# Optimization experiments

Hardware: AMD Instinct MI355X
Metric: run time of the kernel (lower is better)

Reference implementation:

```python
import jax, jax.numpy as jnp
import numpy as np

V = 1.0e10           # large init value for non-seed pixels (FastGeodis v)
LAMB = 0.0           # lamb=0 => pure Euclidean raster-scan distance
ITERS = 2            # FastGeodis iterations
THRESH = 0.7         # binarize_map threshold
TOPO_WEIGHT = 0.005
TOPO_WINDOW = 64
EPS = 1e-6
BIG = 1e20


def _sweep_down(dist, image):
    # One top-down raster sweep of the FastGeodis up-down pass.
    # dist, image: [H, W]. Row r updates from row r-1 at col offsets {-1,0,+1}
    # with squared spatial distances {2,1,2}; lamb weights the intensity term.
    W = dist.shape[1]
    sp2 = (2.0, 1.0, 2.0)

    def step(carry, xs):
        pd, pi = carry          # previous-row distance / intensity, [W]
        d_row, i_row = xs
        pd_pad = jnp.pad(pd, 1, constant_values=BIG)
        pi_pad = jnp.pad(pi, 1, constant_values=0.0)
        new = d_row
        for k in range(3):
            p = pd_pad[k:k + W]
            q = i_row - pi_pad[k:k + W]
            new = jnp.minimum(new, p + jnp.sqrt(sp2[k] + LAMB * q * q))
        return (new, i_row), new

    (_, _), rest = jax.lax.scan(step, (dist[0], image[0]), (dist[1:], image[1:]))
    return jnp.concatenate([dist[:1], rest], axis=0)


def _updown(dist, image):
    dist = _sweep_down(dist, image)
    dist = _sweep_down(dist[::-1], image[::-1])[::-1]
    return dist


def generalised_geodesic2d(image, softmask):
    # image: intensity map [H,W]; softmask: [H,W]; dist init = V * softmask.
    dist = V * softmask
    for _ in range(ITERS):
        dist = _updown(dist, image)
        dist = _updown(dist.T, image.T).T
    return dist


def calculate_edt(inp):
    # Original: softmask = inp, intensity image = 1 - inp (mask_pt = 1 - image_pt).
    return generalised_geodesic2d(1.0 - inp, inp)


def _global_norm(x):
    return (x - x.min()) / (x.max() - x.min() + EPS)


def _topo_loss(p, t, window):
    # Persistence-style matching proxy: within each non-overlapping window,
    # match level-set values of pred and target by sorting (0-dim persistence
    # birth/death values of the filtration are order statistics of the window)
    # and penalize squared differences of matched values.
    H, W = p.shape
    nh, nw = H // window, W // window

    def win_sort(x):
        x = x.reshape(nh, window, nw, window).transpose(0, 2, 1, 3)
        return jnp.sort(x.reshape(nh * nw, window * window), axis=-1)

    return jnp.mean((win_sort(p) - win_sort(t)) ** 2)


def _per_item(pred_i, target_i):
    # pred_i/target_i: [C, H, W]; pred already remapped to [0, 1]
    bin_pred = (pred_i >= THRESH).astype(jnp.float32)
    comb_pred = jnp.max(bin_pred, axis=0)        # combine_channels
    comb_tgt = jnp.max(target_i, axis=0)
    edt_p = _global_norm(calculate_edt(1.0 - comb_pred))
    edt_t = _global_norm(calculate_edt(1.0 - comb_tgt))
    return _topo_loss(edt_p, edt_t, TOPO_WINDOW)


def setup_inputs():
    key = jax.random.key(0)
    k1, k2 = jax.random.split(key)
    B, C, H, W = 16, 3, 512, 512
    pred = jax.random.normal(k1, (B, C, H, W), dtype=jnp.float32)  # model output in ~[-1,1]
    # target: binary multi-channel cell masks (sparse foreground)
    target = (jax.random.uniform(k2, (B, C, H, W)) > 0.8).astype(jnp.float32)
    return {"pred": pred, "target": target}


def reference(pred, target):
    pred01 = (pred + 1.0) / 2.0
    losses = jax.vmap(_per_item)(pred01.astype(jnp.float32), target.astype(jnp.float32))
    mean_loss = losses.mean()
    return (mean_loss * TOPO_WEIGHT, mean_loss)
```

## Files before the change

kernel.cpp:

```cpp
#include <hip/hip_runtime.h>

#define BIGF 1e20f
#define VF   1e10f

constexpr float SQ2 = 1.41421356237309515f;

__device__ __forceinline__ float dpp_left(float x)
{
    int o = __builtin_amdgcn_update_dpp(0x60AD78ECu , __float_as_int(x),
                                        0x138, 0xF, 0xF, false);
    return __int_as_float(o);
}
__device__ __forceinline__ float dpp_right(float x)
{
    int o = __builtin_amdgcn_update_dpp(0x60AD78ECu , __float_as_int(x),
                                        0x130, 0xF, 0xF, false);
    return __int_as_float(o);
}
template<int CTRL>
__device__ __forceinline__ float qdpp(float x)
{
    return __int_as_float(__builtin_amdgcn_update_dpp(0, __float_as_int(x),
                                                      CTRL, 0xF, 0xF, true));
}
__device__ __forceinline__ float fmed3(float a, float b, float c)
{
    return __builtin_amdgcn_fmed3f(a, b, c);
}

__device__ __forceinline__ void load_row8(const float* __restrict__ M, int r, int c0, float v[8])
{
    const float4* q = (const float4*)(M + ((long)r << 9) + c0);
    float4 a = q[0], b = q[1];
    v[0] = a.x; v[1] = a.y; v[2] = a.z; v[3] = a.w;
    v[4] = b.x; v[5] = b.y; v[6] = b.z; v[7] = b.w;
}
__device__ __forceinline__ void store_row8(float* __restrict__ M, int r, int c0, const float v[8])
{
    float4* q = (float4*)(M + ((long)r << 9) + c0);
    q[0] = make_float4(v[0], v[1], v[2], v[3]);
    q[1] = make_float4(v[4], v[5], v[6], v[7]);
}

__device__ __forceinline__ void step8(const float cur[8], const float p[8], float nv[8])
{
    float left  = dpp_left(p[7]);
    float right = dpp_right(p[0]);
    #pragma unroll
    for (int j = 0; j < 8; ++j) {
        float l  = (j == 0) ? left  : p[j - 1];
        float rr = (j == 7) ? right : p[j + 1];
        nv[j] = fminf(fminf(cur[j], p[j] + 1.0f), fminf(l, rr) + SQ2);
    }
}

__global__ __launch_bounds__(256) void k_init(const float* __restrict__ pred,
                                              const float* __restrict__ tgt,
                                              float* __restrict__ bufA,
                                              float* __restrict__ acc,
                                              unsigned* __restrict__ count,
                                              float* __restrict__ minmax)
{
    if (blockIdx.x == 0 && threadIdx.x == 0) { *acc = 0.0f; *count = 0u; }
    if (blockIdx.x == 0 && threadIdx.x < 64)
        minmax[threadIdx.x] = (threadIdx.x & 1) ? 0.0f : BIGF;

    int r = blockIdx.x & 7;
    int k = blockIdx.x >> 3;
    int b = r + 8 * (k >> 10);
    int pix = (k & 1023) * 256 + threadIdx.x;
    long base = (long)b * 3 * 262144 + pix;

    float p0 = pred[base], p1 = pred[base + 262144], p2 = pred[base + 2 * 262144];
    bool fgP = ((p0 + 1.0f) * 0.5f >= 0.7f) ||
               ((p1 + 1.0f) * 0.5f >= 0.7f) ||
               ((p2 + 1.0f) * 0.5f >= 0.7f);

    float t0 = tgt[base], t1 = tgt[base + 262144], t2 = tgt[base + 2 * 262144];
    float mt = fmaxf(fmaxf(t0, t1), t2);

    bufA[(long)b * 262144 + pix]        = fgP ? 0.0f : VF;
    bufA[(long)(16 + b) * 262144 + pix] = VF * (1.0f - mt);
}

__global__ __launch_bounds__(64) void k_p1d(const float* __restrict__ X0,
                                            float* __restrict__ Cb)
{
    int bi = blockIdx.x, m = bi >> 4, w = bi & 15;
    const float* X = X0 + ((long)m << 18);
    int c0 = (int)threadIdx.x << 3, a = w << 5;
    float p[8]; load_row8(X, a, c0, p);
    float buf[8][8];
    #pragma unroll
    for (int k = 1; k <= 7; ++k) load_row8(X, a + k, c0, buf[k & 7]);
    #pragma unroll
    for (int i = 1; i < 32; ++i) {
        if (i + 7 < 32) load_row8(X, a + i + 7, c0, buf[(i + 7) & 7]);
        float nv[8]; step8(buf[i & 7], p, nv);
        #pragma unroll
        for (int j = 0; j < 8; ++j) p[j] = nv[j];
    }
    float4* o = (float4*)(Cb + m * 8192 + w * 512 + c0);
    o[0] = make_float4(p[0], p[1], p[2], p[3]);
    o[1] = make_float4(p[4], p[5], p[6], p[7]);
}

__device__ __forceinline__ void combine(float* __restrict__ bwp, float* __restrict__ part,
                                        int wdst, int wsrc, int t, int wave, int lane,
                                        const float wreg[8])
{
    const float* bs = bwp + wsrc * 576;
    if (wave <= 8) {
        int base = lane * 8 + 8 * wave;
        float W[16];
        float4 W0 = *(const float4*)(bs + base);
        float4 W1 = *(const float4*)(bs + base + 4);
        W[0]=W0.x; W[1]=W0.y; W[2]=W0.z; W[3]=W0.w;
        W[4]=W1.x; W[5]=W1.y; W[6]=W1.z; W[7]=W1.w;
        float acc[8];
        if (wave < 8) {
            float4 W2 = *(const float4*)(bs + base + 8);
            float4 W3 = *(const float4*)(bs + base + 12);
            W[8]=W2.x; W[9]=W2.y; W[10]=W2.z; W[11]=W2.w;
            W[12]=W3.x; W[13]=W3.y; W[14]=W3.z; W[15]=W3.w;
            #pragma unroll
            for (int j = 0; j < 8; ++j) acc[j] = W[j] + wreg[0];
            #pragma unroll
            for (int dt = 1; dt < 8; ++dt)
                #pragma unroll
                for (int j = 0; j < 8; ++j)
                    acc[j] = fminf(acc[j], W[j + dt] + wreg[dt]);
        } else {
            #pragma unroll
            for (int j = 0; j < 8; ++j) acc[j] = W[j] + wreg[0];
        }
        float4* pp = (float4*)(part + wave * 512 + lane * 8);
        pp[0] = make_float4(acc[0], acc[1], acc[2], acc[3]);
        pp[1] = make_float4(acc[4], acc[5], acc[6], acc[7]);
    }
    __syncthreads();
    if (t < 512) {
        float r = bwp[wdst * 576 + 32 + t];
        #pragma unroll
        for (int p2 = 0; p2 < 9; ++p2) r = fminf(r, part[p2 * 512 + t]);
        bwp[wdst * 576 + 32 + t] = r;
    }
    __syncthreads();
}

__global__ __launch_bounds__(1024) void k_comb(float* __restrict__ Cb, int dir)
{
    __shared__ __align__(16) float bwp[16 * 576];
    __shared__ __align__(16) float part[9 * 512];
    __shared__ float wgt[72];
    int m = blockIdx.x, t = threadIdx.x, wave = t >> 6, lane = t & 63, c0 = lane << 3;
    float* Cm = Cb + m * 8192;

    bwp[wave * 576 + ((lane < 32) ? lane : lane + 512)] = BIGF;
    *(float4*)(bwp + wave * 576 + 32 + c0)     = *(const float4*)(Cm + wave * 512 + c0);
    *(float4*)(bwp + wave * 576 + 32 + c0 + 4) = *(const float4*)(Cm + wave * 512 + c0 + 4);
    if (t < 65) { int d = t - 32; int ad = d < 0 ? -d : d; wgt[t] = ad * SQ2 + (float)(32 - ad); }
    __syncthreads();
    float wreg[8];
    #pragma unroll
    for (int dt = 0; dt < 8; ++dt) wreg[dt] = BIGF;
    if (wave < 8) {
        #pragma unroll
        for (int dt = 0; dt < 8; ++dt) wreg[dt] = wgt[wave * 8 + dt];
    } else if (wave == 8) wreg[0] = wgt[64];

    #pragma unroll 1
    for (int i = 0; i < 15; ++i) {
        int w2 = (dir > 0) ? (1 + i) : (14 - i);
        combine(bwp, part, w2, w2 - dir, t, wave, lane, wreg);
    }
    *(float4*)(Cm + wave * 512 + c0)     = *(const float4*)(bwp + wave * 576 + 32 + c0);
    *(float4*)(Cm + wave * 512 + c0 + 4) = *(const float4*)(bwp + wave * 576 + 32 + c0 + 4);
}

__global__ __launch_bounds__(64) void k_p3d1u(const float* __restrict__ X0,
                                              float* __restrict__ Y0,
                                              const float* __restrict__ Cb,
                                              float* __restrict__ Db)
{
    __shared__ __align__(16) float stash[31 * 512];
    int bi = blockIdx.x, m = bi >> 4, w = bi & 15;
    const float* X = X0 + ((long)m << 18);
    float* Y = Y0 + ((long)m << 18);
    const int L = threadIdx.x;
    int c0 = L << 3, a = w << 5;
    float p[8], buf[8][8];

    if (w == 0) {
        load_row8(X, 0, c0, p);
        store_row8(Y, 0, c0, p);
        *(float4*)(stash + 0 * 512 + L * 4)       = make_float4(p[0], p[1], p[2], p[3]);
        *(float4*)(stash + 0 * 512 + 256 + L * 4) = make_float4(p[4], p[5], p[6], p[7]);
        #pragma unroll
        for (int k = 1; k <= 7; ++k) load_row8(X, k, c0, buf[k & 7]);
        #pragma unroll
        for (int i = 1; i < 32; ++i) {
            if (i + 7 < 32) load_row8(X, i + 7, c0, buf[(i + 7) & 7]);
            float nv[8]; step8(buf[i & 7], p, nv);
            store_row8(Y, i, c0, nv);
            if (i < 31) {
                *(float4*)(stash + i * 512 + L * 4)       = make_float4(nv[0], nv[1], nv[2], nv[3]);
                *(float4*)(stash + i * 512 + 256 + L * 4) = make_float4(nv[4], nv[5], nv[6], nv[7]);
            }
            #pragma unroll
            for (int j = 0; j < 8; ++j) p[j] = nv[j];
        }
    } else {
        const float4* s = (const float4*)(Cb + m * 8192 + (w - 1) * 512 + c0);
        float4 s0 = s[0], s1 = s[1];
        p[0]=s0.x; p[1]=s0.y; p[2]=s0.z; p[3]=s0.w;
        p[4]=s1.x; p[5]=s1.y; p[6]=s1.z; p[7]=s1.w;
        #pragma unroll
        for (int k = 0; k < 7; ++k) load_row8(X, a + k, c0, buf[k & 7]);
        #pragma unroll
        for (int i = 0; i < 32; ++i) {
            if (i + 7 < 32) load_row8(X, a + i + 7, c0, buf[(i + 7) & 7]);
            float nv[8]; step8(buf[i & 7], p, nv);
            store_row8(Y, a + i, c0, nv);
            if (i < 31) {
                *(float4*)(stash + i * 512 + L * 4)       = make_float4(nv[0], nv[1], nv[2], nv[3]);
                *(float4*)(stash + i * 512 + 256 + L * 4) = make_float4(nv[4], nv[5], nv[6], nv[7]);
            }
            #pragma unroll
            for (int j = 0; j < 8; ++j) p[j] = nv[j];
        }
    }

    float q[8], cur[8];
    #pragma unroll
    for (int j = 0; j < 8; ++j) q[j] = p[j];
    {
        float4 x0 = *(const float4*)(stash + 30 * 512 + L * 4);
        float4 x1 = *(const float4*)(stash + 30 * 512 + 256 + L * 4);
        cur[0]=x0.x; cur[1]=x0.y; cur[2]=x0.z; cur[3]=x0.w;
        cur[4]=x1.x; cur[5]=x1.y; cur[6]=x1.z; cur[7]=x1.w;
    }
    #pragma unroll
    for (int i = 1; i < 32; ++i) {
        float nxt[8];
        if (i < 31) {
            float4 x0 = *(const float4*)(stash + (30 - i) * 512 + L * 4);
            float4 x1 = *(const float4*)(stash + (30 - i) * 512 + 256 + L * 4);
            nxt[0]=x0.x; nxt[1]=x0.y; nxt[2]=x0.z; nxt[3]=x0.w;
            nxt[4]=x1.x; nxt[5]=x1.y; nxt[6]=x1.z; nxt[7]=x1.w;
        }
        float nv[8]; step8(cur, q, nv);
        #pragma unroll
        for (int j = 0; j < 8; ++j) q[j] = nv[j];
        if (i < 31) {
            #pragma unroll
            for (int j = 0; j < 8; ++j) cur[j] = nxt[j];
        }
    }
    float4* o = (float4*)(Db + m * 8192 + w * 512 + c0);
    o[0] = make_float4(q[0], q[1], q[2], q[3]);
    o[1] = make_float4(q[4], q[5], q[6], q[7]);
}

__device__ __forceinline__ void tile_store(float* tile, int h, int c0, const float v[8])
{
    float4* q = (float4*)(tile + h * 516 + c0);
    q[0] = make_float4(v[0], v[1], v[2], v[3]);
    q[1] = make_float4(v[4], v[5], v[6], v[7]);
}
__device__ __forceinline__ void half_out(const float* tile, float* __restrict__ Xo,
                                         int a2, int L)
{
    int g = L >> 2, j = (L & 3) << 2;
    #pragma unroll
    for (int it = 0; it < 32; ++it) {
        int c = (it << 4) + g;
        float4 v = make_float4(tile[(j + 0) * 516 + c], tile[(j + 1) * 516 + c],
                               tile[(j + 2) * 516 + c], tile[(j + 3) * 516 + c]);
        *(float4*)(Xo + (long)c * 512 + a2 + j) = v;
    }
}

__global__ __launch_bounds__(64) void k_p3u(const float* __restrict__ Y0,
                                            float* __restrict__ Xo0,
                                            const float* __restrict__ Db,
                                            float* __restrict__ minmax,
                                            int final_pass)
{
    __shared__ __align__(16) float tile[16 * 516];
    int bi = blockIdx.x, m = bi >> 4, w = bi & 15;
    const float* Y = Y0 + ((long)m << 18);
    float* Xo = Xo0 + ((long)m << 18);
    int L = threadIdx.x, c0 = L << 3, a = w << 5;
    float p[8], buf[8][8];
    float mn = BIGF, mx = -BIGF;

    if (w == 15) {
        load_row8(Y, 511, c0, p);
        tile_store(tile, 15, c0, p);
        #pragma unroll
        for (int j = 0; j < 8; ++j) { mn = fminf(mn, p[j]); mx = fmaxf(mx, p[j]); }
        #pragma unroll
        for (int k = 1; k <= 7; ++k) load_row8(Y, 511 - k, c0, buf[k & 7]);
        #pragma unroll
        for (int i = 1; i < 16; ++i) {
            if (i + 7 < 32) load_row8(Y, 511 - (i + 7), c0, buf[(i + 7) & 7]);
            float nv[8]; step8(buf[i & 7], p, nv);
            tile_store(tile, 15 - i, c0, nv);
            #pragma unroll
            for (int j = 0; j < 8; ++j) { p[j] = nv[j]; mn = fminf(mn, nv[j]); mx = fmaxf(mx, nv[j]); }
        }
        half_out(tile, Xo, a + 16, L);
        #pragma unroll
        for (int i = 16; i < 32; ++i) {
            if (i + 7 < 32) load_row8(Y, 511 - (i + 7), c0, buf[(i + 7) & 7]);
            float nv[8]; step8(buf[i & 7], p, nv);
            tile_store(tile, 31 - i, c0, nv);
            #pragma unroll
            for (int j = 0; j < 8; ++j) { p[j] = nv[j]; mn = fminf(mn, nv[j]); mx = fmaxf(mx, nv[j]); }
        }
        half_out(tile, Xo, a, L);
    } else {
        const float4* s = (const float4*)(Db + m * 8192 + (w + 1) * 512 + c0);
        float4 s0 = s[0], s1 = s[1];
        p[0]=s0.x; p[1]=s0.y; p[2]=s0.z; p[3]=s0.w;
        p[4]=s1.x; p[5]=s1.y; p[6]=s1.z; p[7]=s1.w;
        #pragma unroll
        for (int k = 0; k < 7; ++k) load_row8(Y, a + 31 - k, c0, buf[k & 7]);
        #pragma unroll
        for (int i = 0; i < 16; ++i) {
            if (i + 7 < 32) load_row8(Y, a + 31 - (i + 7), c0, buf[(i + 7) & 7]);
            float nv[8]; step8(buf[i & 7], p, nv);
            tile_store(tile, 15 - i, c0, nv);
            #pragma unroll
            for (int j = 0; j < 8; ++j) { p[j] = nv[j]; mn = fminf(mn, nv[j]); mx = fmaxf(mx, nv[j]); }
        }
        half_out(tile, Xo, a + 16, L);
        #pragma unroll
        for (int i = 16; i < 32; ++i) {
            if (i + 7 < 32) load_row8(Y, a + 31 - (i + 7), c0, buf[(i + 7) & 7]);
            float nv[8]; step8(buf[i & 7], p, nv);
            tile_store(tile, 31 - i, c0, nv);
            #pragma unroll
            for (int j = 0; j < 8; ++j) { p[j] = nv[j]; mn = fminf(mn, nv[j]); mx = fmaxf(mx, nv[j]); }
        }
        half_out(tile, Xo, a, L);
    }

    if (final_pass) {
        for (int o = 32; o > 0; o >>= 1) {
            mn = fminf(mn, __shfl_down(mn, o));
            mx = fmaxf(mx, __shfl_down(mx, o));
        }
        if (L == 0) {
            atomicMin((int*)(minmax + 2 * m),     __float_as_int(mn));
            atomicMax((int*)(minmax + 2 * m + 1), __float_as_int(mx));
        }
    }
}

__device__ __forceinline__ void cex(float& lo, float& hi)
{
    float l = fminf(lo, hi);
    hi = fmaxf(lo, hi);
    lo = l;
}
__device__ __forceinline__ void merge8asc(float v[8])
{
    cex(v[0],v[4]); cex(v[1],v[5]); cex(v[2],v[6]); cex(v[3],v[7]);
    cex(v[0],v[2]); cex(v[1],v[3]); cex(v[4],v[6]); cex(v[5],v[7]);
    cex(v[0],v[1]); cex(v[2],v[3]); cex(v[4],v[5]); cex(v[6],v[7]);
}
__device__ __forceinline__ void sort8asc(float v[8])
{
    cex(v[0],v[1]); cex(v[2],v[3]); cex(v[4],v[5]); cex(v[6],v[7]);
    cex(v[0],v[3]); cex(v[1],v[2]); cex(v[4],v[7]); cex(v[5],v[6]);
    cex(v[0],v[1]); cex(v[2],v[3]); cex(v[4],v[5]); cex(v[6],v[7]);
    cex(v[0],v[7]); cex(v[1],v[6]); cex(v[2],v[5]); cex(v[3],v[4]);
    cex(v[0],v[2]); cex(v[1],v[3]); cex(v[4],v[6]); cex(v[5],v[7]);
    cex(v[0],v[1]); cex(v[2],v[3]); cex(v[4],v[5]); cex(v[6],v[7]);
}
__device__ __forceinline__ void xshfl(float v[8], int j8, float sel)
{
    #pragma unroll
    for (int e = 0; e < 8; ++e) {
        float o = __shfl_xor(v[e], j8);
        v[e] = fmed3(v[e], o, sel);
    }
}
template<int CTRL>
__device__ __forceinline__ void xdpp(float v[8], float sel)
{
    #pragma unroll
    for (int e = 0; e < 8; ++e) {
        float o = qdpp<CTRL>(v[e]);
        v[e] = fmed3(v[e], o, sel);
    }
}
__device__ __forceinline__ void rshfl(float v[8], int tmask, float sel)
{
    float o[8];
    #pragma unroll
    for (int e = 0; e < 8; ++e) o[e] = __shfl_xor(v[7 - e], tmask);
    #pragma unroll
    for (int e = 0; e < 8; ++e) v[e] = fmed3(v[e], o[e], sel);
}
template<int CTRL>
__device__ __forceinline__ void rdpp(float v[8], float sel)
{
    float o[8];
    #pragma unroll
    for (int e = 0; e < 8; ++e) o[e] = qdpp<CTRL>(v[7 - e]);
    #pragma unroll
    for (int e = 0; e < 8; ++e) v[e] = fmed3(v[e], o[e], sel);
}
__device__ __forceinline__ void lstage(float p[8], float q[8], int tmask, float sel, bool rev,
                                       float* sp, float* st, int t)
{
    __syncthreads();
    int sw = (t >> 2) & 1;
    int o0 = t * 8 + sw * 4;
    int o1 = t * 8 + (sw ^ 1) * 4;
    *(float4*)(sp + o0) = make_float4(p[0], p[1], p[2], p[3]);
    *(float4*)(sp + o1) = make_float4(p[4], p[5], p[6], p[7]);
    *(float4*)(st + o0) = make_float4(q[0], q[1], q[2], q[3]);
    *(float4*)(st + o1) = make_float4(q[4], q[5], q[6], q[7]);
    __syncthreads();
    int pt = t ^ tmask;
    int psw = (pt >> 2) & 1;
    int q0 = pt * 8 + psw * 4;
    int q1 = pt * 8 + (psw ^ 1) * 4;
    float4 a = *(const float4*)(sp + q0), bb = *(const float4*)(sp + q1);
    float4 c = *(const float4*)(st + q0), d = *(const float4*)(st + q1);
    float op[8] = {a.x,a.y,a.z,a.w,bb.x,bb.y,bb.z,bb.w};
    float oq[8] = {c.x,c.y,c.z,c.w,d.x,d.y,d.z,d.w};
    if (rev) {
        #pragma unroll
        for (int e = 0; e < 8; ++e) {
            p[e] = fmed3(p[e], op[7 - e], sel);
            q[e] = fmed3(q[e], oq[7 - e], sel);
        }
    } else {
        #pragma unroll
        for (int e = 0; e < 8; ++e) {
            p[e] = fmed3(p[e], op[e], sel);
            q[e] = fmed3(q[e], oq[e], sel);
        }
    }
}

__global__ __launch_bounds__(512) void k_loss(const float* __restrict__ bufB,
                                              const float* __restrict__ minmax,
                                              float* __restrict__ acc,
                                              unsigned* __restrict__ count,
                                              float* __restrict__ out)
{
    __shared__ float sp[4096];
    __shared__ float st[4096];
    __shared__ float rs[8];

    int t = threadIdx.x;
    int r = blockIdx.x & 7;
    int k = blockIdx.x >> 3;
    int b = r + 8 * (k >> 6);
    int w = k & 63;
    int wi = w >> 3, wj = w & 7;

    int i0 = t << 3;
    int y = wi * 64 + (i0 >> 6);
    int x = wj * 64 + (i0 & 63);

    float mnP = minmax[2 * b],        mxP = minmax[2 * b + 1];
    float mnT = minmax[2 * (16 + b)], mxT = minmax[2 * (16 + b) + 1];
    float sclP = 1.0f / (mxP - mnP + 1e-6f);
    float sclT = 1.0f / (mxT - mnT + 1e-6f);

    float p[8], q[8];
    {
        const float4* P4 = (const float4*)(bufB + (long)b * 262144 + y * 512 + x);
        const float4* T4 = (const float4*)(bufB + (long)(16 + b) * 262144 + y * 512 + x);
        float4 a = P4[0], bb = P4[1], c = T4[0], d = T4[1];
        p[0]=a.x; p[1]=a.y; p[2]=a.z; p[3]=a.w; p[4]=bb.x; p[5]=bb.y; p[6]=bb.z; p[7]=bb.w;
        q[0]=c.x; q[1]=c.y; q[2]=c.z; q[3]=c.w; q[4]=d.x;  q[5]=d.y;  q[6]=d.z;  q[7]=d.w;
        #pragma unroll
        for (int e = 0; e < 8; ++e) {
            p[e] = (p[e] - mnP) * sclP;
            q[e] = (q[e] - mnT) * sclT;
        }
    }

    const float INFP = __builtin_inff();
    sort8asc(p); sort8asc(q);

    #pragma unroll 1
    for (int kk = 16; kk <= 4096; kk <<= 1) {
        int tmask = (kk - 1) >> 3;
        float sel = ((t & (kk >> 4)) == 0) ? -INFP : INFP;
        if (kk == 16)        { rdpp<0xB1>(p, sel); rdpp<0xB1>(q, sel); }
        else if (kk == 32)   { rdpp<0x1B>(p, sel); rdpp<0x1B>(q, sel); }
        else if (tmask < 64) { rshfl(p, tmask, sel); rshfl(q, tmask, sel); }
        else                 lstage(p, q, tmask, sel, true, sp, st, t);

        #pragma unroll 1
        for (int j = kk >> 2; j >= 8; j >>= 1) {
            int j8 = j >> 3;
            float s2 = ((t & j8) == 0) ? -INFP : INFP;
            if (j8 == 1)      { xdpp<0xB1>(p, s2); xdpp<0xB1>(q, s2); }
            else if (j8 == 2) { xdpp<0x4E>(p, s2); xdpp<0x4E>(q, s2); }
            else if (j8 < 64) { xshfl(p, j8, s2); xshfl(q, j8, s2); }
            else              lstage(p, q, j8, s2, false, sp, st, t);
        }
        merge8asc(p); merge8asc(q);
    }

    float s = 0.0f;
    #pragma unroll
    for (int e = 0; e < 8; ++e) { float d = p[e] - q[e]; s += d * d; }
    for (int o = 32; o > 0; o >>= 1) s += __shfl_down(s, o);
    if ((t & 63) == 0) rs[t >> 6] = s;
    __syncthreads();
    if (t == 0) {
        float tot = 0.0f;
        #pragma unroll
        for (int i = 0; i < 8; ++i) tot += rs[i];
        atomicAdd(acc, tot);
        __threadfence();
        unsigned done = atomicAdd(count, 1u);
        if (done == 1023u) {
            float total = atomicAdd(acc, 0.0f);
            float mean = total * (1.0f / 4194304.0f);
            out[0] = mean * 0.005f;
            out[1] = mean;
        }
    }
}

extern "C" void kernel_launch(void* const* d_in, const int* in_sizes, int n_in,
                              void* d_out, int out_size, void* d_ws, size_t ws_size,
                              hipStream_t stream)
{
    const float* pred = (const float*)d_in[0];
    const float* tgt  = (const float*)d_in[1];
    float* out = (float*)d_out;

    char* ws = (char*)d_ws;
    float* bufA     = (float*)ws;
    float* bufB     = (float*)(ws + (32ull << 20));
    float* Cb       = (float*)(ws + (64ull << 20));
    float* Db       = (float*)(ws + (65ull << 20));
    float* minmax   = (float*)(ws + (66ull << 20));
    float* acc      = minmax + 64;
    unsigned* count = (unsigned*)(acc + 1);

    k_init<<<16 * 1024, 256, 0, stream>>>(pred, tgt, bufA, acc, count, minmax);

    for (int s = 0; s < 4; ++s) {
        k_p1d  <<<512,   64, 0, stream>>>(bufA, Cb);
        k_comb <<< 32, 1024, 0, stream>>>(Cb, +1);
        k_p3d1u<<<512,   64, 0, stream>>>(bufA, bufB, Cb, Db);
        k_comb <<< 32, 1024, 0, stream>>>(Db, -1);
        k_p3u  <<<512,   64, 0, stream>>>(bufB, bufA, Db, minmax, s == 3 ? 1 : 0);
    }

    k_loss<<<1024, 512, 0, stream>>>(bufA, minmax, acc, count, out);
}
```

Measured before the change: 406.6 us.

## Split sweep kernels into column quarters with halo columns to quadruple block count

The p3d1u and p3u sweep kernels now split each 512-column strip into four 128-column pieces, each computed by one 64-lane wave with a 32-column halo on each side. Because a 32-row sweep spreads dependence by at most one column per row, the halo makes each piece exact. Launches grow from 512 to 2048 blocks to raise occupancy on the many CUs, and shared-memory tiles shrink. The cost is redundant halo computation, scalar (non-vectorized) loads in p3u, and partially wasted lanes.

```diff
diff --git a/kernel.cpp b/kernel.cpp
--- a/kernel.cpp
+++ b/kernel.cpp
@@ -35,12 +35,6 @@
     v[0] = a.x; v[1] = a.y; v[2] = a.z; v[3] = a.w;
     v[4] = b.x; v[5] = b.y; v[6] = b.z; v[7] = b.w;
 }
-__device__ __forceinline__ void store_row8(float* __restrict__ M, int r, int c0, const float v[8])
-{
-    float4* q = (float4*)(M + ((long)r << 9) + c0);
-    q[0] = make_float4(v[0], v[1], v[2], v[3]);
-    q[1] = make_float4(v[4], v[5], v[6], v[7]);
-}
 
 __device__ __forceinline__ void step8(const float cur[8], const float p[8], float nv[8])
 {
@@ -52,6 +46,24 @@
         float rr = (j == 7) ? right : p[j + 1];
         nv[j] = fminf(fminf(cur[j], p[j] + 1.0f), fminf(l, rr) + SQ2);
     }
+}
+
+__device__ __forceinline__ void step3(const float cur[3], const float p[3], float nv[3])
+{
+    float left  = dpp_left(p[2]);
+    float right = dpp_right(p[0]);
+    nv[0] = fminf(fminf(cur[0], p[0] + 1.0f), fminf(left, p[1]) + SQ2);
+    nv[1] = fminf(fminf(cur[1], p[1] + 1.0f), fminf(p[0], p[2]) + SQ2);
+    nv[2] = fminf(fminf(cur[2], p[2] + 1.0f), fminf(p[1], right) + SQ2);
+}
+__device__ __forceinline__ void step4(const float cur[4], const float p[4], float nv[4])
+{
+    float left  = dpp_left(p[3]);
+    float right = dpp_right(p[0]);
+    nv[0] = fminf(fminf(cur[0], p[0] + 1.0f), fminf(left, p[1]) + SQ2);
+    nv[1] = fminf(fminf(cur[1], p[1] + 1.0f), fminf(p[0], p[2]) + SQ2);
+    nv[2] = fminf(fminf(cur[2], p[2] + 1.0f), fminf(p[1], p[3]) + SQ2);
+    nv[3] = fminf(fminf(cur[3], p[3] + 1.0f), fminf(p[2], right) + SQ2);
 }
 
 __global__ __launch_bounds__(256) void k_init(const float* __restrict__ pred,
@@ -183,101 +195,83 @@
                                               const float* __restrict__ Cb,
                                               float* __restrict__ Db)
 {
-    __shared__ __align__(16) float stash[31 * 512];
-    int bi = blockIdx.x, m = bi >> 4, w = bi & 15;
+    __shared__ __align__(16) float stash[32 * 192];
+    int bi = blockIdx.x;
+    int u = bi & 3, w = (bi >> 2) & 15, m = bi >> 6;
     const float* X = X0 + ((long)m << 18);
     float* Y = Y0 + ((long)m << 18);
-    const int L = threadIdx.x;
-    int c0 = L << 3, a = w << 5;
-    float p[8], buf[8][8];
-
-    if (w == 0) {
-        load_row8(X, 0, c0, p);
-        store_row8(Y, 0, c0, p);
-        *(float4*)(stash + 0 * 512 + L * 4)       = make_float4(p[0], p[1], p[2], p[3]);
-        *(float4*)(stash + 0 * 512 + 256 + L * 4) = make_float4(p[4], p[5], p[6], p[7]);
-        #pragma unroll
-        for (int k = 1; k <= 7; ++k) load_row8(X, k, c0, buf[k & 7]);
-        #pragma unroll
-        for (int i = 1; i < 32; ++i) {
-            if (i + 7 < 32) load_row8(X, i + 7, c0, buf[(i + 7) & 7]);
-            float nv[8]; step8(buf[i & 7], p, nv);
-            store_row8(Y, i, c0, nv);
-            if (i < 31) {
-                *(float4*)(stash + i * 512 + L * 4)       = make_float4(nv[0], nv[1], nv[2], nv[3]);
-                *(float4*)(stash + i * 512 + 256 + L * 4) = make_float4(nv[4], nv[5], nv[6], nv[7]);
-            }
-            #pragma unroll
-            for (int j = 0; j < 8; ++j) p[j] = nv[j];
-        }
-    } else {
-        const float4* s = (const float4*)(Cb + m * 8192 + (w - 1) * 512 + c0);
-        float4 s0 = s[0], s1 = s[1];
-        p[0]=s0.x; p[1]=s0.y; p[2]=s0.z; p[3]=s0.w;
-        p[4]=s1.x; p[5]=s1.y; p[6]=s1.z; p[7]=s1.w;
-        #pragma unroll
-        for (int k = 0; k < 7; ++k) load_row8(X, a + k, c0, buf[k & 7]);
-        #pragma unroll
-        for (int i = 0; i < 32; ++i) {
-            if (i + 7 < 32) load_row8(X, a + i + 7, c0, buf[(i + 7) & 7]);
-            float nv[8]; step8(buf[i & 7], p, nv);
-            store_row8(Y, a + i, c0, nv);
-            if (i < 31) {
-                *(float4*)(stash + i * 512 + L * 4)       = make_float4(nv[0], nv[1], nv[2], nv[3]);
-                *(float4*)(stash + i * 512 + 256 + L * 4) = make_float4(nv[4], nv[5], nv[6], nv[7]);
-            }
-            #pragma unroll
-            for (int j = 0; j < 8; ++j) p[j] = nv[j];
-        }
-    }
-
-    float q[8], cur[8];
-    #pragma unroll
-    for (int j = 0; j < 8; ++j) q[j] = p[j];
-    {
-        float4 x0 = *(const float4*)(stash + 30 * 512 + L * 4);
-        float4 x1 = *(const float4*)(stash + 30 * 512 + 256 + L * 4);
-        cur[0]=x0.x; cur[1]=x0.y; cur[2]=x0.z; cur[3]=x0.w;
-        cur[4]=x1.x; cur[5]=x1.y; cur[6]=x1.z; cur[7]=x1.w;
-    }
+    const int ln = threadIdx.x;
+    const int a = w << 5;
+    const int c4 = (u << 7) - 64 + (ln << 2);
+    const bool inb = (unsigned)c4 < 512u;
+    const bool own4 = (ln >= 16) && (ln < 48);
+    const bool st4  = (ln >= 8)  && (ln < 56);
+    const int sidx = (ln << 2) - 32;
+
+    float p[4], buf[8][4];
+    if (w) {
+        if (inb) {
+            float4 s = *(const float4*)(Cb + m * 8192 + (w - 1) * 512 + c4);
+            p[0]=s.x; p[1]=s.y; p[2]=s.z; p[3]=s.w;
+        } else { p[0]=p[1]=p[2]=p[3]=BIGF; }
+    } else { p[0]=p[1]=p[2]=p[3]=BIGF; }
+
+    #pragma unroll
+    for (int k = 0; k < 7; ++k) {
+        if (inb) {
+            float4 v = *(const float4*)(X + ((long)(a + k) << 9) + c4);
+            buf[k][0]=v.x; buf[k][1]=v.y; buf[k][2]=v.z; buf[k][3]=v.w;
+        } else { buf[k][0]=buf[k][1]=buf[k][2]=buf[k][3]=BIGF; }
+    }
+    #pragma unroll
+    for (int i = 0; i < 32; ++i) {
+        if (i + 7 < 32) {
+            int s = (i + 7) & 7;
+            if (inb) {
+                float4 v = *(const float4*)(X + ((long)(a + i + 7) << 9) + c4);
+                buf[s][0]=v.x; buf[s][1]=v.y; buf[s][2]=v.z; buf[s][3]=v.w;
+            } else { buf[s][0]=buf[s][1]=buf[s][2]=buf[s][3]=BIGF; }
+        }
+        float nv[4]; step4(buf[i & 7], p, nv);
+        if (own4)
+            *(float4*)(Y + ((long)(a + i) << 9) + c4) = make_float4(nv[0], nv[1], nv[2], nv[3]);
+        if (st4)
+            *(float4*)(stash + i * 192 + sidx) = make_float4(nv[0], nv[1], nv[2], nv[3]);
+        p[0]=nv[0]; p[1]=nv[1]; p[2]=nv[2]; p[3]=nv[3];
+    }
+
+    const int t3 = ln * 3;
+    float q[3];
+    q[0] = stash[31 * 192 + t3];
+    q[1] = stash[31 * 192 + t3 + 1];
+    q[2] = stash[31 * 192 + t3 + 2];
     #pragma unroll
     for (int i = 1; i < 32; ++i) {
-        float nxt[8];
-        if (i < 31) {
-            float4 x0 = *(const float4*)(stash + (30 - i) * 512 + L * 4);
-            float4 x1 = *(const float4*)(stash + (30 - i) * 512 + 256 + L * 4);
-            nxt[0]=x0.x; nxt[1]=x0.y; nxt[2]=x0.z; nxt[3]=x0.w;
-            nxt[4]=x1.x; nxt[5]=x1.y; nxt[6]=x1.z; nxt[7]=x1.w;
-        }
-        float nv[8]; step8(cur, q, nv);
-        #pragma unroll
-        for (int j = 0; j < 8; ++j) q[j] = nv[j];
-        if (i < 31) {
-            #pragma unroll
-            for (int j = 0; j < 8; ++j) cur[j] = nxt[j];
-        }
-    }
-    float4* o = (float4*)(Db + m * 8192 + w * 512 + c0);
-    o[0] = make_float4(q[0], q[1], q[2], q[3]);
-    o[1] = make_float4(q[4], q[5], q[6], q[7]);
-}
-
-__device__ __forceinline__ void tile_store(float* tile, int h, int c0, const float v[8])
-{
-    float4* q = (float4*)(tile + h * 516 + c0);
-    q[0] = make_float4(v[0], v[1], v[2], v[3]);
-    q[1] = make_float4(v[4], v[5], v[6], v[7]);
-}
-__device__ __forceinline__ void half_out(const float* tile, float* __restrict__ Xo,
-                                         int a2, int L)
-{
-    int g = L >> 2, j = (L & 3) << 2;
-    #pragma unroll
-    for (int it = 0; it < 32; ++it) {
+        float cur[3];
+        cur[0] = stash[(31 - i) * 192 + t3];
+        cur[1] = stash[(31 - i) * 192 + t3 + 1];
+        cur[2] = stash[(31 - i) * 192 + t3 + 2];
+        float nv[3]; step3(cur, q, nv);
+        q[0]=nv[0]; q[1]=nv[1]; q[2]=nv[2];
+    }
+    float* Drow = Db + m * 8192 + w * 512;
+    #pragma unroll
+    for (int e = 0; e < 3; ++e) {
+        int t = t3 + e;
+        if (t >= 32 && t < 160) Drow[(u << 7) + t - 32] = q[e];
+    }
+}
+
+__device__ __forceinline__ void half_out3(const float* tile, float* __restrict__ Xo,
+                                          int cbase, int a2, int ln)
+{
+    int g = ln >> 2, j = (ln & 3) << 2;
+    #pragma unroll
+    for (int it = 0; it < 8; ++it) {
         int c = (it << 4) + g;
-        float4 v = make_float4(tile[(j + 0) * 516 + c], tile[(j + 1) * 516 + c],
-                               tile[(j + 2) * 516 + c], tile[(j + 3) * 516 + c]);
-        *(float4*)(Xo + (long)c * 512 + a2 + j) = v;
+        float4 v = make_float4(tile[(j + 0) * 132 + c], tile[(j + 1) * 132 + c],
+                               tile[(j + 2) * 132 + c], tile[(j + 3) * 132 + c]);
+        *(float4*)(Xo + (long)(cbase + c) * 512 + a2 + j) = v;
     }
 }
 
@@ -287,72 +281,83 @@
                                             float* __restrict__ minmax,
                                             int final_pass)
 {
-    __shared__ __align__(16) float tile[16 * 516];
-    int bi = blockIdx.x, m = bi >> 4, w = bi & 15;
+    __shared__ __align__(16) float tile[16 * 132];
+    int bi = blockIdx.x;
+    int u = bi & 3, w = (bi >> 2) & 15, m = bi >> 6;
     const float* Y = Y0 + ((long)m << 18);
     float* Xo = Xo0 + ((long)m << 18);
-    int L = threadIdx.x, c0 = L << 3, a = w << 5;
-    float p[8], buf[8][8];
+    const int ln = threadIdx.x;
+    const int a = w << 5;
+    const int cb = (u << 7) - 32 + ln * 3;
+    bool ok[3], own[3]; int oc[3];
+    #pragma unroll
+    for (int e = 0; e < 3; ++e) {
+        int c = cb + e;
+        ok[e]  = (unsigned)c < 512u;
+        oc[e]  = c - (u << 7);
+        own[e] = (oc[e] >= 0) && (oc[e] < 128);
+    }
+
+    float p[3], buf[8][3];
+    if (w < 15) {
+        const float* S = Db + m * 8192 + (w + 1) * 512;
+        p[0] = ok[0] ? S[cb    ] : BIGF;
+        p[1] = ok[1] ? S[cb + 1] : BIGF;
+        p[2] = ok[2] ? S[cb + 2] : BIGF;
+    } else { p[0]=p[1]=p[2]=BIGF; }
+
+    #pragma unroll
+    for (int k = 0; k < 7; ++k) {
+        const float* Yr = Y + ((long)(a + 31 - k) << 9);
+        buf[k][0] = ok[0] ? Yr[cb    ] : BIGF;
+        buf[k][1] = ok[1] ? Yr[cb + 1] : BIGF;
+        buf[k][2] = ok[2] ? Yr[cb + 2] : BIGF;
+    }
+
     float mn = BIGF, mx = -BIGF;
-
-    if (w == 15) {
-        load_row8(Y, 511, c0, p);
-        tile_store(tile, 15, c0, p);
-        #pragma unroll
-        for (int j = 0; j < 8; ++j) { mn = fminf(mn, p[j]); mx = fmaxf(mx, p[j]); }
-        #pragma unroll
-        for (int k = 1; k <= 7; ++k) load_row8(Y, 511 - k, c0, buf[k & 7]);
-        #pragma unroll
-        for (int i = 1; i < 16; ++i) {
-            if (i + 7 < 32) load_row8(Y, 511 - (i + 7), c0, buf[(i + 7) & 7]);
-            float nv[8]; step8(buf[i & 7], p, nv);
-            tile_store(tile, 15 - i, c0, nv);
-            #pragma unroll
-            for (int j = 0; j < 8; ++j) { p[j] = nv[j]; mn = fminf(mn, nv[j]); mx = fmaxf(mx, nv[j]); }
-        }
-        half_out(tile, Xo, a + 16, L);
-        #pragma unroll
-        for (int i = 16; i < 32; ++i) {
-            if (i + 7 < 32) load_row8(Y, 511 - (i + 7), c0, buf[(i + 7) & 7]);
-            float nv[8]; step8(buf[i & 7], p, nv);
-            tile_store(tile, 31 - i, c0, nv);
-            #pragma unroll
-            for (int j = 0; j < 8; ++j) { p[j] = nv[j]; mn = fminf(mn, nv[j]); mx = fmaxf(mx, nv[j]); }
-        }
-        half_out(tile, Xo, a, L);
-    } else {
-        const float4* s = (const float4*)(Db + m * 8192 + (w + 1) * 512 + c0);
-        float4 s0 = s[0], s1 = s[1];
-        p[0]=s0.x; p[1]=s0.y; p[2]=s0.z; p[3]=s0.w;
-        p[4]=s1.x; p[5]=s1.y; p[6]=s1.z; p[7]=s1.w;
-        #pragma unroll
-        for (int k = 0; k < 7; ++k) load_row8(Y, a + 31 - k, c0, buf[k & 7]);
-        #pragma unroll
-        for (int i = 0; i < 16; ++i) {
-            if (i + 7 < 32) load_row8(Y, a + 31 - (i + 7), c0, buf[(i + 7) & 7]);
-            float nv[8]; step8(buf[i & 7], p, nv);
-            tile_store(tile, 15 - i, c0, nv);
-            #pragma unroll
-            for (int j = 0; j < 8; ++j) { p[j] = nv[j]; mn = fminf(mn, nv[j]); mx = fmaxf(mx, nv[j]); }
-        }
-        half_out(tile, Xo, a + 16, L);
-        #pragma unroll
-        for (int i = 16; i < 32; ++i) {
-            if (i + 7 < 32) load_row8(Y, a + 31 - (i + 7), c0, buf[(i + 7) & 7]);
-            float nv[8]; step8(buf[i & 7], p, nv);
-            tile_store(tile, 31 - i, c0, nv);
-            #pragma unroll
-            for (int j = 0; j < 8; ++j) { p[j] = nv[j]; mn = fminf(mn, nv[j]); mx = fmaxf(mx, nv[j]); }
-        }
-        half_out(tile, Xo, a, L);
-    }
+    #pragma unroll
+    for (int i = 0; i < 16; ++i) {
+        {
+            const float* Yr = Y + ((long)(a + 31 - (i + 7)) << 9);
+            buf[(i + 7) & 7][0] = ok[0] ? Yr[cb    ] : BIGF;
+            buf[(i + 7) & 7][1] = ok[1] ? Yr[cb + 1] : BIGF;
+            buf[(i + 7) & 7][2] = ok[2] ? Yr[cb + 2] : BIGF;
+        }
+        float nv[3]; step3(buf[i & 7], p, nv);
+        #pragma unroll
+        for (int e = 0; e < 3; ++e)
+            if (own[e]) {
+                tile[(15 - i) * 132 + oc[e]] = nv[e];
+                mn = fminf(mn, nv[e]); mx = fmaxf(mx, nv[e]);
+            }
+        p[0]=nv[0]; p[1]=nv[1]; p[2]=nv[2];
+    }
+    half_out3(tile, Xo, u << 7, a + 16, ln);
+    #pragma unroll
+    for (int i = 16; i < 32; ++i) {
+        if (i + 7 < 32) {
+            const float* Yr = Y + ((long)(a + 31 - (i + 7)) << 9);
+            buf[(i + 7) & 7][0] = ok[0] ? Yr[cb    ] : BIGF;
+            buf[(i + 7) & 7][1] = ok[1] ? Yr[cb + 1] : BIGF;
+            buf[(i + 7) & 7][2] = ok[2] ? Yr[cb + 2] : BIGF;
+        }
+        float nv[3]; step3(buf[i & 7], p, nv);
+        #pragma unroll
+        for (int e = 0; e < 3; ++e)
+            if (own[e]) {
+                tile[(31 - i) * 132 + oc[e]] = nv[e];
+                mn = fminf(mn, nv[e]); mx = fmaxf(mx, nv[e]);
+            }
+        p[0]=nv[0]; p[1]=nv[1]; p[2]=nv[2];
+    }
+    half_out3(tile, Xo, u << 7, a, ln);
 
     if (final_pass) {
         for (int o = 32; o > 0; o >>= 1) {
             mn = fminf(mn, __shfl_down(mn, o));
             mx = fmaxf(mx, __shfl_down(mx, o));
         }
-        if (L == 0) {
+        if (ln == 0) {
             atomicMin((int*)(minmax + 2 * m),     __float_as_int(mn));
             atomicMax((int*)(minmax + 2 * m + 1), __float_as_int(mx));
         }
@@ -555,11 +560,11 @@
     k_init<<<16 * 1024, 256, 0, stream>>>(pred, tgt, bufA, acc, count, minmax);
 
     for (int s = 0; s < 4; ++s) {
-        k_p1d  <<<512,   64, 0, stream>>>(bufA, Cb);
-        k_comb <<< 32, 1024, 0, stream>>>(Cb, +1);
-        k_p3d1u<<<512,   64, 0, stream>>>(bufA, bufB, Cb, Db);
-        k_comb <<< 32, 1024, 0, stream>>>(Db, -1);
-        k_p3u  <<<512,   64, 0, stream>>>(bufB, bufA, Db, minmax, s == 3 ? 1 : 0);
+        k_p1d  <<< 512,   64, 0, stream>>>(bufA, Cb);
+        k_comb <<<  32, 1024, 0, stream>>>(Cb, +1);
+        k_p3d1u<<<2048,   64, 0, stream>>>(bufA, bufB, Cb, Db);
+        k_comb <<<  32, 1024, 0, stream>>>(Db, -1);
+        k_p3u  <<<2048,   64, 0, stream>>>(bufB, bufA, Db, minmax, s == 3 ? 1 : 0);
     }
 
     k_loss<<<1024, 512, 0, stream>>>(bufA, minmax, acc, count, out);
```

Result: slower. 497.9 us (+22.5%).
